# Performance work log

Hardware: AMD Instinct MI355X
Metric: run time of the kernel (lower is better)

Reference implementation:

```python
import jax, jax.numpy as jnp
import numpy as np

B, T, C, H = 256, 256, 512, 64  # batch, seq, n_embd, head_size


def setup_inputs() -> dict:
    key = jax.random.key(0)
    kx, kk, kq, kv = jax.random.split(key, 4)
    x = jax.random.normal(kx, (B, T, C), dtype=jnp.float32)
    # nn.Linear(C, H, bias=False): store as [C, H] so y = x @ W
    Wk = jax.random.normal(kk, (C, H), dtype=jnp.float32) * (C ** -0.5)
    Wq = jax.random.normal(kq, (C, H), dtype=jnp.float32) * (C ** -0.5)
    Wv = jax.random.normal(kv, (C, H), dtype=jnp.float32) * (C ** -0.5)
    return {"x": x, "Wk": Wk, "Wq": Wq, "Wv": Wv}


def reference(x, Wk, Wq, Wv):
    Bx, Tx, Cx = x.shape
    k = jnp.einsum('btc,ch->bth', x, Wk)
    q = jnp.einsum('btc,ch->bth', x, Wq)
    v = jnp.einsum('btc,ch->bth', x, Wv)
    # NOTE: original scales by C**-0.5 (embed dim), not head_size**-0.5
    wei = jnp.einsum('bth,bsh->bts', q, k) * (Cx ** -0.5)  # [B,T,T]
    causal = jnp.tril(jnp.ones((Tx, Tx), dtype=bool))
    wei = jnp.where(causal, wei, -jnp.inf)
    wei = jax.nn.softmax(wei, axis=-1)
    # dropout is identity at inference (deterministic reference)
    out = jnp.einsum('bts,bsh->bth', wei, v)  # [B,T,H]
    return out
```

## Files before the change

### kernel.cpp

```cpp
#include <hip/hip_runtime.h>

#define BB 256
#define TT 256
#define CC 512
#define HH 64

typedef __bf16 bf16;
typedef __bf16 bf16x4 __attribute__((ext_vector_type(4)));
typedef __bf16 bf16x8 __attribute__((ext_vector_type(8)));
typedef float  f32x4  __attribute__((ext_vector_type(4)));

#define MFMA16(a, b, c) __builtin_amdgcn_mfma_f32_16x16x32_bf16((a), (b), (c), 0, 0, 0)

typedef __attribute__((address_space(1))) const void cas1_void;
typedef __attribute__((address_space(3))) void as3_void;
__device__ __forceinline__ void g2lds16(const void* g, void* l) {
    __builtin_amdgcn_global_load_lds((cas1_void*)g, (as3_void*)l, 16, 0, 0);
}

__global__ __launch_bounds__(256) void wtrans(const float* __restrict__ Wk,
                                              const float* __restrict__ Wq,
                                              const float* __restrict__ Wv,
                                              bf16* __restrict__ wt) {
    int which = blockIdx.y;
    const float* W = (which == 0) ? Wq : (which == 1) ? Wk : Wv;
    int idx = blockIdx.x * 256 + threadIdx.x;
    int n = idx & 63, k4 = idx >> 6;
    bf16x4 o;
    #pragma unroll
    for (int i = 0; i < 4; ++i) o[i] = (bf16)W[(k4 * 4 + i) * HH + n];
    *(bf16x4*)(&wt[which * (CC * HH) + n * CC + k4 * 4]) = o;
}

__global__ __launch_bounds__(512, 2) void fused(const float* __restrict__ x,
                                                const bf16* __restrict__ wt,
                                                float* __restrict__ out) {
    __shared__ __align__(16) char smem[131072];
    const int tid  = threadIdx.x;
    const int wv   = tid >> 6;
    const int lane = tid & 63;
    const int quad = lane >> 4;
    const int l15  = lane & 15;
    const int l7   = l15 & 7;
    const int l3   = l15 & 3;
    const int b    = blockIdx.x;
    const float* xg = x + (size_t)b * TT * CC;

    auto stage = [&](int p, int kc) {
        char* xbase = smem + p * 32768;
        #pragma unroll
        for (int j = 0; j < 4; ++j) {
            int s = j * 512 + tid;
            int r = s >> 3, up = s & 7;
            int u = up ^ (r & 7);
            const float* gp = xg + (size_t)r * CC + kc * 32 + u * 4;
            g2lds16(gp, xbase + (j * 512 + wv * 64) * 16);
        }
        if (wv < 6) {
            char* wbase = smem + 65536 + p * 12288;
            #pragma unroll
            for (int j = 0; j < 2; ++j) {
                int n = wv * 32 + j * 16 + (lane >> 2);
                int u = (lane & 3) ^ (n & 3);
                const bf16* gp = wt + (size_t)n * CC + kc * 32 + u * 8;
                g2lds16(gp, wbase + (wv * 32 + j * 16) * 64);
            }
        }
    };

    f32x4 acc[2][12];
    #pragma unroll
    for (int mt = 0; mt < 2; ++mt)
        #pragma unroll
        for (int nt = 0; nt < 12; ++nt)
            acc[mt][nt] = (f32x4){0.f, 0.f, 0.f, 0.f};

    stage(0, 0);
    __syncthreads();

    for (int kc = 0; kc < 16; ++kc) {
        int p = kc & 1;
        if (kc < 15) stage(p ^ 1, kc + 1);

        const char* xbase = smem + p * 32768;
        const char* wbase = smem + 65536 + p * 12288;
        #pragma unroll
        for (int mt = 0; mt < 2; ++mt) {
            int row = wv * 32 + mt * 16 + l15;
            const char* rp = xbase + row * 128;
            f32x4 x0 = *(const f32x4*)(rp + (((quad * 2)     ^ l7) * 16));
            f32x4 x1 = *(const f32x4*)(rp + (((quad * 2 + 1) ^ l7) * 16));
            bf16x8 a0;
            #pragma unroll
            for (int j = 0; j < 4; ++j) {
                a0[j] = (bf16)x0[j]; a0[j + 4] = (bf16)x1[j];
            }
            #pragma unroll
            for (int nt = 0; nt < 12; ++nt) {
                int n = (nt >> 2) * 64 + (nt & 3) * 16 + l15;
                const char* np = wbase + n * 64;
                bf16x8 b0 = *(const bf16x8*)(np + ((quad ^ l3) * 16));
                acc[mt][nt] = MFMA16(a0, b0, acc[mt][nt]);
            }
        }
        __syncthreads();
    }

    bf16* qs = (bf16*)smem;
    bf16* ks = (bf16*)(smem + 32768);
    bf16* vs = (bf16*)(smem + 65536);
    const float scale = 0.044194173824159216f;
    #pragma unroll
    for (int mt = 0; mt < 2; ++mt) {
        int gt = wv * 32 + mt * 16 + quad * 4;
        #pragma unroll
        for (int nt = 0; nt < 12; ++nt) {
            int h = (nt & 3) * 16 + l15;
            int wch = nt >> 2;
            if (wch == 0) {
                #pragma unroll
                for (int r = 0; r < 4; ++r) {
                    int row = gt + r;
                    *(bf16*)((char*)qs + row * 128 + (((h >> 3) ^ (row & 7)) * 16)
                             + (h & 7) * 2) = (bf16)(acc[mt][nt][r] * scale);
                }
            } else if (wch == 1) {
                #pragma unroll
                for (int r = 0; r < 4; ++r) {
                    int row = gt + r;
                    *(bf16*)((char*)ks + row * 128 + (((h >> 3) ^ (row & 7)) * 16)
                             + (h & 7) * 2) = (bf16)(acc[mt][nt][r]);
                }
            } else {
                bf16x4 pv;
                #pragma unroll
                for (int r = 0; r < 4; ++r) pv[r] = (bf16)(acc[mt][nt][r]);
                *(bf16x4*)((char*)vs + h * 512 + (((gt >> 3) ^ (h & 31)) * 16)
                           + ((gt >> 2) & 1) * 8) = pv;
            }
        }
    }
    __syncthreads();

    bf16* pb = (bf16*)(smem + 98304 + wv * 4096);

    #pragma unroll
    for (int ti = 0; ti < 2; ++ti) {
        const int rt = (ti == 0) ? wv : (15 - wv);
        const int rowbase = rt * 16;
        const int ctmax = rt;

        const int qr = rowbase + l15;
        const char* qp = (const char*)qs + qr * 128;
        bf16x8 bq0 = *(const bf16x8*)(qp + ((quad ^ l7) * 16));
        bf16x8 bq1 = *(const bf16x8*)(qp + (((4 + quad) ^ l7) * 16));

        f32x4 sv[16];
        #pragma unroll
        for (int ct = 0; ct < 16; ++ct) {
            if (ct <= ctmax) {
                const char* kp = (const char*)ks + (ct * 16 + l15) * 128;
                bf16x8 k0 = *(const bf16x8*)(kp + ((quad ^ l7) * 16));
                bf16x8 k1 = *(const bf16x8*)(kp + (((4 + quad) ^ l7) * 16));
                f32x4 a = (f32x4){0.f, 0.f, 0.f, 0.f};
                a = MFMA16(k0, bq0, a);
                a = MFMA16(k1, bq1, a);
                int t = rowbase + l15;
                #pragma unroll
                for (int r = 0; r < 4; ++r) {
                    int s = ct * 16 + quad * 4 + r;
                    sv[ct][r] = (s <= t) ? a[r] : -3.0e38f;
                }
            }
        }

        float mx = -3.0e38f;
        #pragma unroll
        for (int ct = 0; ct < 16; ++ct)
            if (ct <= ctmax) {
                #pragma unroll
                for (int r = 0; r < 4; ++r) mx = fmaxf(mx, sv[ct][r]);
            }
        mx = fmaxf(mx, __shfl_xor(mx, 16));
        mx = fmaxf(mx, __shfl_xor(mx, 32));

        float sm = 0.f;
        f32x4 o[4];
        #pragma unroll
        for (int ht = 0; ht < 4; ++ht) o[ht] = (f32x4){0.f, 0.f, 0.f, 0.f};

        #pragma unroll
        for (int hp = 0; hp < 2; ++hp) {
            if (hp * 8 <= ctmax) {
                #pragma unroll
                for (int c2 = 0; c2 < 8; ++c2) {
                    int ct = hp * 8 + c2;
                    if (ct <= ctmax) {
                        bf16x4 ev;
                        #pragma unroll
                        for (int r = 0; r < 4; ++r) {
                            float e = __expf(sv[ct][r] - mx);
                            sm += e;
                            ev[r] = (bf16)e;
                        }
                        int u = 2 * c2 + (quad >> 1);
                        *(bf16x4*)((char*)pb + l15 * 256 + ((u ^ l15) * 16)
                                   + (quad & 1) * 8) = ev;
                    }
                }
                if (ctmax >= hp * 8 && ctmax < hp * 8 + 8 && !(ctmax & 1)) {
                    int c2z = (ctmax & 7) + 1;
                    int u = 2 * c2z + (quad >> 1);
                    *(bf16x4*)((char*)pb + l15 * 256 + ((u ^ l15) * 16)
                               + (quad & 1) * 8) =
                        (bf16x4){(bf16)0.f, (bf16)0.f, (bf16)0.f, (bf16)0.f};
                }
                asm volatile("" ::: "memory");

                #pragma unroll
                for (int k2 = 0; k2 < 4; ++k2) {
                    int ks2 = hp * 4 + k2;
                    if (ks2 <= (ctmax >> 1)) {
                        int ur = 4 * k2 + quad;
                        bf16x8 pf = *(const bf16x8*)((char*)pb + l15 * 256
                                                     + ((ur ^ l15) * 16));
                        #pragma unroll
                        for (int ht = 0; ht < 4; ++ht) {
                            int vr = ht * 16 + l15;
                            bf16x8 vf = *(const bf16x8*)((const char*)vs + vr * 512
                                         + (((ks2 * 4 + quad) ^ (vr & 31)) * 16));
                            o[ht] = MFMA16(vf, pf, o[ht]);
                        }
                    }
                }
                asm volatile("" ::: "memory");
            }
        }
        sm += __shfl_xor(sm, 16);
        sm += __shfl_xor(sm, 32);

        float rinv = 1.0f / sm;
        int t = rowbase + l15;
        #pragma unroll
        for (int ht = 0; ht < 4; ++ht) {
            f32x4 ov;
            #pragma unroll
            for (int r = 0; r < 4; ++r) ov[r] = o[ht][r] * rinv;
            *(f32x4*)(&out[((size_t)b * TT + t) * HH + ht * 16 + quad * 4]) = ov;
        }
        asm volatile("" ::: "memory");
    }
}

extern "C" void kernel_launch(void* const* d_in, const int* in_sizes, int n_in,
                              void* d_out, int out_size, void* d_ws, size_t ws_size,
                              hipStream_t stream) {
    const float* x  = (const float*)d_in[0];
    const float* Wk = (const float*)d_in[1];
    const float* Wq = (const float*)d_in[2];
    const float* Wv = (const float*)d_in[3];

    bf16* wt = (bf16*)d_ws;
    float* out = (float*)d_out;

    wtrans<<<dim3(32, 3), 256, 0, stream>>>(Wk, Wq, Wv, wt);
    fused<<<dim3(256), 512, 0, stream>>>(x, wt, out);
}
```

Before: 210.9 us.

## Use 1024-thread blocks with one row tile per wave and online softmax

```diff
diff --git a/kernel.cpp b/kernel.cpp
--- a/kernel.cpp
+++ b/kernel.cpp
@@ -32,9 +32,9 @@
     *(bf16x4*)(&wt[which * (CC * HH) + n * CC + k4 * 4]) = o;
 }
 
-__global__ __launch_bounds__(512, 2) void fused(const float* __restrict__ x,
-                                                const bf16* __restrict__ wt,
-                                                float* __restrict__ out) {
+__global__ __launch_bounds__(1024) void fused(const float* __restrict__ x,
+                                              const bf16* __restrict__ wt,
+                                              float* __restrict__ out) {
     __shared__ __align__(16) char smem[131072];
     const int tid  = threadIdx.x;
     const int wv   = tid >> 6;
@@ -49,31 +49,25 @@
     auto stage = [&](int p, int kc) {
         char* xbase = smem + p * 32768;
         #pragma unroll
-        for (int j = 0; j < 4; ++j) {
-            int s = j * 512 + tid;
+        for (int j = 0; j < 2; ++j) {
+            int s = j * 1024 + tid;
             int r = s >> 3, up = s & 7;
             int u = up ^ (r & 7);
             const float* gp = xg + (size_t)r * CC + kc * 32 + u * 4;
-            g2lds16(gp, xbase + (j * 512 + wv * 64) * 16);
-        }
-        if (wv < 6) {
+            g2lds16(gp, xbase + (j * 1024 + wv * 64) * 16);
+        }
+        if (wv < 12) {
             char* wbase = smem + 65536 + p * 12288;
-            #pragma unroll
-            for (int j = 0; j < 2; ++j) {
-                int n = wv * 32 + j * 16 + (lane >> 2);
-                int u = (lane & 3) ^ (n & 3);
-                const bf16* gp = wt + (size_t)n * CC + kc * 32 + u * 8;
-                g2lds16(gp, wbase + (wv * 32 + j * 16) * 64);
-            }
+            int n = wv * 16 + (lane >> 2);
+            int u = (lane & 3) ^ (n & 3);
+            const bf16* gp = wt + (size_t)n * CC + kc * 32 + u * 8;
+            g2lds16(gp, wbase + wv * 1024);
         }
     };
 
-    f32x4 acc[2][12];
-    #pragma unroll
-    for (int mt = 0; mt < 2; ++mt)
-        #pragma unroll
-        for (int nt = 0; nt < 12; ++nt)
-            acc[mt][nt] = (f32x4){0.f, 0.f, 0.f, 0.f};
+    f32x4 acc[12];
+    #pragma unroll
+    for (int nt = 0; nt < 12; ++nt) acc[nt] = (f32x4){0.f, 0.f, 0.f, 0.f};
 
     stage(0, 0);
     __syncthreads();
@@ -84,24 +78,21 @@
 
         const char* xbase = smem + p * 32768;
         const char* wbase = smem + 65536 + p * 12288;
-        #pragma unroll
-        for (int mt = 0; mt < 2; ++mt) {
-            int row = wv * 32 + mt * 16 + l15;
-            const char* rp = xbase + row * 128;
-            f32x4 x0 = *(const f32x4*)(rp + (((quad * 2)     ^ l7) * 16));
-            f32x4 x1 = *(const f32x4*)(rp + (((quad * 2 + 1) ^ l7) * 16));
-            bf16x8 a0;
-            #pragma unroll
-            for (int j = 0; j < 4; ++j) {
-                a0[j] = (bf16)x0[j]; a0[j + 4] = (bf16)x1[j];
-            }
-            #pragma unroll
-            for (int nt = 0; nt < 12; ++nt) {
-                int n = (nt >> 2) * 64 + (nt & 3) * 16 + l15;
-                const char* np = wbase + n * 64;
-                bf16x8 b0 = *(const bf16x8*)(np + ((quad ^ l3) * 16));
-                acc[mt][nt] = MFMA16(a0, b0, acc[mt][nt]);
-            }
+        int row = wv * 16 + l15;
+        const char* rp = xbase + row * 128;
+        f32x4 x0 = *(const f32x4*)(rp + (((quad * 2)     ^ l7) * 16));
+        f32x4 x1 = *(const f32x4*)(rp + (((quad * 2 + 1) ^ l7) * 16));
+        bf16x8 a0;
+        #pragma unroll
+        for (int j = 0; j < 4; ++j) {
+            a0[j] = (bf16)x0[j]; a0[j + 4] = (bf16)x1[j];
+        }
+        #pragma unroll
+        for (int nt = 0; nt < 12; ++nt) {
+            int n = (nt >> 2) * 64 + (nt & 3) * 16 + l15;
+            const char* np = wbase + n * 64;
+            bf16x8 b0 = *(const bf16x8*)(np + ((quad ^ l3) * 16));
+            acc[nt] = MFMA16(a0, b0, acc[nt]);
         }
         __syncthreads();
     }
@@ -110,9 +101,8 @@
     bf16* ks = (bf16*)(smem + 32768);
     bf16* vs = (bf16*)(smem + 65536);
     const float scale = 0.044194173824159216f;
-    #pragma unroll
-    for (int mt = 0; mt < 2; ++mt) {
-        int gt = wv * 32 + mt * 16 + quad * 4;
+    {
+        int gt = wv * 16 + quad * 4;
         #pragma unroll
         for (int nt = 0; nt < 12; ++nt) {
             int h = (nt & 3) * 16 + l15;
@@ -122,19 +112,19 @@
                 for (int r = 0; r < 4; ++r) {
                     int row = gt + r;
                     *(bf16*)((char*)qs + row * 128 + (((h >> 3) ^ (row & 7)) * 16)
-                             + (h & 7) * 2) = (bf16)(acc[mt][nt][r] * scale);
+                             + (h & 7) * 2) = (bf16)(acc[nt][r] * scale);
                 }
             } else if (wch == 1) {
                 #pragma unroll
                 for (int r = 0; r < 4; ++r) {
                     int row = gt + r;
                     *(bf16*)((char*)ks + row * 128 + (((h >> 3) ^ (row & 7)) * 16)
-                             + (h & 7) * 2) = (bf16)(acc[mt][nt][r]);
+                             + (h & 7) * 2) = (bf16)(acc[nt][r]);
                 }
             } else {
                 bf16x4 pv;
                 #pragma unroll
-                for (int r = 0; r < 4; ++r) pv[r] = (bf16)(acc[mt][nt][r]);
+                for (int r = 0; r < 4; ++r) pv[r] = (bf16)(acc[nt][r]);
                 *(bf16x4*)((char*)vs + h * 512 + (((gt >> 3) ^ (h & 31)) * 16)
                            + ((gt >> 2) & 1) * 8) = pv;
             }
@@ -142,113 +132,115 @@
     }
     __syncthreads();
 
-    bf16* pb = (bf16*)(smem + 98304 + wv * 4096);
-
-    #pragma unroll
-    for (int ti = 0; ti < 2; ++ti) {
-        const int rt = (ti == 0) ? wv : (15 - wv);
-        const int rowbase = rt * 16;
-        const int ctmax = rt;
-
-        const int qr = rowbase + l15;
-        const char* qp = (const char*)qs + qr * 128;
-        bf16x8 bq0 = *(const bf16x8*)(qp + ((quad ^ l7) * 16));
-        bf16x8 bq1 = *(const bf16x8*)(qp + (((4 + quad) ^ l7) * 16));
-
-        f32x4 sv[16];
-        #pragma unroll
-        for (int ct = 0; ct < 16; ++ct) {
-            if (ct <= ctmax) {
-                const char* kp = (const char*)ks + (ct * 16 + l15) * 128;
-                bf16x8 k0 = *(const bf16x8*)(kp + ((quad ^ l7) * 16));
-                bf16x8 k1 = *(const bf16x8*)(kp + (((4 + quad) ^ l7) * 16));
-                f32x4 a = (f32x4){0.f, 0.f, 0.f, 0.f};
-                a = MFMA16(k0, bq0, a);
-                a = MFMA16(k1, bq1, a);
-                int t = rowbase + l15;
-                #pragma unroll
-                for (int r = 0; r < 4; ++r) {
-                    int s = ct * 16 + quad * 4 + r;
-                    sv[ct][r] = (s <= t) ? a[r] : -3.0e38f;
-                }
-            }
-        }
-
-        float mx = -3.0e38f;
-        #pragma unroll
-        for (int ct = 0; ct < 16; ++ct)
-            if (ct <= ctmax) {
-                #pragma unroll
-                for (int r = 0; r < 4; ++r) mx = fmaxf(mx, sv[ct][r]);
-            }
-        mx = fmaxf(mx, __shfl_xor(mx, 16));
-        mx = fmaxf(mx, __shfl_xor(mx, 32));
-
-        float sm = 0.f;
-        f32x4 o[4];
-        #pragma unroll
-        for (int ht = 0; ht < 4; ++ht) o[ht] = (f32x4){0.f, 0.f, 0.f, 0.f};
-
-        #pragma unroll
-        for (int hp = 0; hp < 2; ++hp) {
-            if (hp * 8 <= ctmax) {
-                #pragma unroll
-                for (int c2 = 0; c2 < 8; ++c2) {
-                    int ct = hp * 8 + c2;
-                    if (ct <= ctmax) {
-                        bf16x4 ev;
-                        #pragma unroll
-                        for (int r = 0; r < 4; ++r) {
-                            float e = __expf(sv[ct][r] - mx);
-                            sm += e;
-                            ev[r] = (bf16)e;
-                        }
-                        int u = 2 * c2 + (quad >> 1);
-                        *(bf16x4*)((char*)pb + l15 * 256 + ((u ^ l15) * 16)
-                                   + (quad & 1) * 8) = ev;
+    bf16* pb = (bf16*)(smem + 98304 + wv * 2048);
+    const int w0 = wv & 1, w1 = (wv >> 1) & 1, w2 = (wv >> 2) & 1, w3 = wv >> 3;
+    const int rt = (w3 << 3) | ((w1 ^ w3) << 2) | (w2 << 1) | (w0 ^ w2);
+    const int rowbase = rt * 16;
+    const int ctmax = rt;
+    const int t = rowbase + l15;
+
+    const char* qp = (const char*)qs + t * 128;
+    bf16x8 bq0 = *(const bf16x8*)(qp + ((quad ^ l7) * 16));
+    bf16x8 bq1 = *(const bf16x8*)(qp + (((4 + quad) ^ l7) * 16));
+
+    float m_run = -3.0e38f, sm = 0.f;
+    f32x4 o[4];
+    #pragma unroll
+    for (int ht = 0; ht < 4; ++ht) o[ht] = (f32x4){0.f, 0.f, 0.f, 0.f};
+
+    #pragma unroll
+    for (int qp4 = 0; qp4 < 4; ++qp4) {
+        if (qp4 * 4 <= ctmax) {
+            f32x4 sv[4];
+            #pragma unroll
+            for (int c2 = 0; c2 < 4; ++c2) {
+                int ct = qp4 * 4 + c2;
+                if (ct <= ctmax) {
+                    const char* kp = (const char*)ks + (ct * 16 + l15) * 128;
+                    bf16x8 k0 = *(const bf16x8*)(kp + ((quad ^ l7) * 16));
+                    bf16x8 k1 = *(const bf16x8*)(kp + (((4 + quad) ^ l7) * 16));
+                    f32x4 a = (f32x4){0.f, 0.f, 0.f, 0.f};
+                    a = MFMA16(k0, bq0, a);
+                    a = MFMA16(k1, bq1, a);
+                    #pragma unroll
+                    for (int r = 0; r < 4; ++r) {
+                        int s = ct * 16 + quad * 4 + r;
+                        sv[c2][r] = (s <= t) ? a[r] : -3.0e38f;
                     }
                 }
-                if (ctmax >= hp * 8 && ctmax < hp * 8 + 8 && !(ctmax & 1)) {
-                    int c2z = (ctmax & 7) + 1;
-                    int u = 2 * c2z + (quad >> 1);
-                    *(bf16x4*)((char*)pb + l15 * 256 + ((u ^ l15) * 16)
-                               + (quad & 1) * 8) =
-                        (bf16x4){(bf16)0.f, (bf16)0.f, (bf16)0.f, (bf16)0.f};
-                }
-                asm volatile("" ::: "memory");
-
-                #pragma unroll
-                for (int k2 = 0; k2 < 4; ++k2) {
-                    int ks2 = hp * 4 + k2;
-                    if (ks2 <= (ctmax >> 1)) {
-                        int ur = 4 * k2 + quad;
-                        bf16x8 pf = *(const bf16x8*)((char*)pb + l15 * 256
-                                                     + ((ur ^ l15) * 16));
-                        #pragma unroll
-                        for (int ht = 0; ht < 4; ++ht) {
-                            int vr = ht * 16 + l15;
-                            bf16x8 vf = *(const bf16x8*)((const char*)vs + vr * 512
-                                         + (((ks2 * 4 + quad) ^ (vr & 31)) * 16));
-                            o[ht] = MFMA16(vf, pf, o[ht]);
-                        }
+            }
+            float mq = -3.0e38f;
+            #pragma unroll
+            for (int c2 = 0; c2 < 4; ++c2)
+                if (qp4 * 4 + c2 <= ctmax) {
+                    #pragma unroll
+                    for (int r = 0; r < 4; ++r) mq = fmaxf(mq, sv[c2][r]);
+                }
+            mq = fmaxf(mq, __shfl_xor(mq, 16));
+            mq = fmaxf(mq, __shfl_xor(mq, 32));
+            float mnew = fmaxf(m_run, mq);
+            float alpha = __expf(m_run - mnew);
+            sm *= alpha;
+            #pragma unroll
+            for (int ht = 0; ht < 4; ++ht)
+                #pragma unroll
+                for (int r = 0; r < 4; ++r) o[ht][r] *= alpha;
+            m_run = mnew;
+
+            #pragma unroll
+            for (int c2 = 0; c2 < 4; ++c2) {
+                int ct = qp4 * 4 + c2;
+                if (ct <= ctmax) {
+                    bf16x4 ev;
+                    #pragma unroll
+                    for (int r = 0; r < 4; ++r) {
+                        float e = __expf(sv[c2][r] - m_run);
+                        sm += e;
+                        ev[r] = (bf16)e;
                     }
-                }
-                asm volatile("" ::: "memory");
-            }
-        }
-        sm += __shfl_xor(sm, 16);
-        sm += __shfl_xor(sm, 32);
-
-        float rinv = 1.0f / sm;
-        int t = rowbase + l15;
-        #pragma unroll
-        for (int ht = 0; ht < 4; ++ht) {
-            f32x4 ov;
-            #pragma unroll
-            for (int r = 0; r < 4; ++r) ov[r] = o[ht][r] * rinv;
-            *(f32x4*)(&out[((size_t)b * TT + t) * HH + ht * 16 + quad * 4]) = ov;
-        }
-        asm volatile("" ::: "memory");
+                    int u = 2 * c2 + (quad >> 1);
+                    *(bf16x4*)((char*)pb + l15 * 128 + ((u ^ l7) * 16)
+                               + (quad & 1) * 8) = ev;
+                }
+            }
+            if (ctmax >= qp4 * 4 && ctmax < qp4 * 4 + 4 && !(ctmax & 1)) {
+                int c2z = (ctmax & 3) + 1;
+                int u = 2 * c2z + (quad >> 1);
+                *(bf16x4*)((char*)pb + l15 * 128 + ((u ^ l7) * 16)
+                           + (quad & 1) * 8) =
+                    (bf16x4){(bf16)0.f, (bf16)0.f, (bf16)0.f, (bf16)0.f};
+            }
+            asm volatile("" ::: "memory");
+
+            #pragma unroll
+            for (int k2 = 0; k2 < 2; ++k2) {
+                int ks2 = qp4 * 2 + k2;
+                if (ks2 <= (ctmax >> 1)) {
+                    int ur = 4 * k2 + quad;
+                    bf16x8 pf = *(const bf16x8*)((char*)pb + l15 * 128
+                                                 + ((ur ^ l7) * 16));
+                    #pragma unroll
+                    for (int ht = 0; ht < 4; ++ht) {
+                        int vr = ht * 16 + l15;
+                        bf16x8 vf = *(const bf16x8*)((const char*)vs + vr * 512
+                                     + (((ks2 * 4 + quad) ^ (vr & 31)) * 16));
+                        o[ht] = MFMA16(vf, pf, o[ht]);
+                    }
+                }
+            }
+            asm volatile("" ::: "memory");
+        }
+    }
+    sm += __shfl_xor(sm, 16);
+    sm += __shfl_xor(sm, 32);
+
+    float rinv = 1.0f / sm;
+    #pragma unroll
+    for (int ht = 0; ht < 4; ++ht) {
+        f32x4 ov;
+        #pragma unroll
+        for (int r = 0; r < 4; ++r) ov[r] = o[ht][r] * rinv;
+        *(f32x4*)(&out[((size_t)b * TT + t) * HH + ht * 16 + quad * 4]) = ov;
     }
 }
 
@@ -264,5 +256,5 @@
     float* out = (float*)d_out;
 
     wtrans<<<dim3(32, 3), 256, 0, stream>>>(Wk, Wq, Wv, wt);
-    fused<<<dim3(256), 512, 0, stream>>>(x, wt, out);
-}
+    fused<<<dim3(256), 1024, 0, stream>>>(x, wt, out);
+}
```

Result: no change. 209.5 us (-0.6%).
